# Kernel tuning notes

Measured on AMD Instinct MI355X. Metric: run time of the kernel, lower is better.

The kernel has to match this reference:

```python
import jax, jax.numpy as jnp
import numpy as np

N_PIECES = 20  # hard-coded in FSEncoderSized.__init__ (FSPool(..., 20))


def conv1x1(x, w, b):
    # x: (B, Cin, N), w: (Cout, Cin), b: (Cout,) -> (B, Cout, N)
    return jnp.einsum('bcn,dc->bdn', x, w) + b[None, :, None]


def fspool(x, weight):
    # x: (B, C, N); weight: (C, N_PIECES+1)
    # FSPool with n=None: sizes = arange(N)/(N-1) clamped to 1, mask all ones.
    B, C, N = x.shape
    ratio = jnp.clip(jnp.arange(N, dtype=jnp.float32) / max(N - 1, 1), 0.0, 1.0)
    pos = N_PIECES * ratio                      # (N,) in [0, N_PIECES]
    idx = jnp.floor(pos).astype(jnp.int32)
    frac = pos - idx
    left = weight[:, idx]                       # (C, N)
    right = weight[:, jnp.clip(idx + 1, 0, N_PIECES)]
    w = (1.0 - frac)[None, :] * left + frac[None, :] * right  # (C, N)
    xs = -jnp.sort(-x, axis=2)                  # descending sort along set dim
    return jnp.sum(xs * w[None], axis=2)        # (B, C)


def setup_inputs() -> dict:
    key = jax.random.key(0)
    ks = jax.random.split(key, 12)
    B, Cin, N = 1024, 5, 512
    dim, Cout = 256, 129
    C = Cout - 1  # 128
    x = jax.random.normal(ks[0], (B, Cin, N), dtype=jnp.float32)
    mask = (jax.random.uniform(ks[1], (B, N)) < 0.8).astype(jnp.float32)

    def kaiming(k, co, ci):
        return jax.random.normal(k, (co, ci), dtype=jnp.float32) * np.sqrt(2.0 / ci)

    w1 = kaiming(ks[2], dim, Cin); b1 = jnp.zeros((dim,), jnp.float32)
    w2 = kaiming(ks[3], dim, dim); b2 = jnp.zeros((dim,), jnp.float32)
    w3 = kaiming(ks[4], dim, dim); b3 = jnp.zeros((dim,), jnp.float32)
    w4 = kaiming(ks[5], C, dim);   b4 = jnp.zeros((C,), jnp.float32)
    pool_w = jax.random.normal(ks[6], (C, N_PIECES + 1), dtype=jnp.float32) * 0.1
    return {'x': x, 'mask': mask, 'w1': w1, 'b1': b1, 'w2': w2, 'b2': b2,
            'w3': w3, 'b3': b3, 'w4': w4, 'b4': b4, 'pool_w': pool_w}


def reference(x, mask, w1, b1, w2, b2, w3, b3, w4, b4, pool_w):
    m = mask[:, None, :]                         # (B, 1, N)
    h = jax.nn.relu(conv1x1(x, w1, b1))
    h = jax.nn.relu(conv1x1(h, w2, b2))
    h = jax.nn.relu(conv1x1(h, w3, b3))
    h = conv1x1(h, w4, b4)                       # (B, C, N)
    h = h / h.shape[2]                           # x / x.size(2)
    h = h * m
    pooled = fspool(h, pool_w)                   # (B, C)
    size_feat = jnp.mean(m, axis=2) * 4.0        # (B, 1)
    return jnp.concatenate([pooled, size_feat], axis=1)  # (B, C+1)
```

## Files before the change

### kernel.cpp

```cpp
#include <hip/hip_runtime.h>
#include <hip/hip_bf16.h>

typedef __bf16 bf16x8 __attribute__((ext_vector_type(8)));
typedef float f32x4 __attribute__((ext_vector_type(4)));
typedef unsigned short ushort_t;

#define NPOS 512
#define CIN  5
#define CO   128

static __device__ __forceinline__ unsigned short f2bf(float f){
  union { __hip_bfloat16 h; unsigned short u; } cv;
  cv.h = __float2bfloat16(f);
  return cv.u;
}

static __device__ __forceinline__ unsigned cvtpk_u32(float a, float b){
  union { __hip_bfloat162 h2; unsigned u; } cv;
  cv.h2 = __float22bfloat162_rn(make_float2(a, b));
  return cv.u;
}

static __device__ __forceinline__ unsigned pk_min_u16(unsigned a, unsigned b){
  unsigned d; asm("v_pk_min_u16 %0, %1, %2" : "=v"(d) : "v"(a), "v"(b)); return d;
}
static __device__ __forceinline__ unsigned pk_max_u16(unsigned a, unsigned b){
  unsigned d; asm("v_pk_max_u16 %0, %1, %2" : "=v"(d) : "v"(a), "v"(b)); return d;
}
static __device__ __forceinline__ unsigned pk_max_i16(unsigned a, unsigned b){
  unsigned d; asm("v_pk_max_i16 %0, %1, %2" : "=v"(d) : "v"(a), "v"(b)); return d;
}

template<int CTRL>
static __device__ __forceinline__ unsigned mov_dpp_u32(unsigned v){
  return (unsigned)__builtin_amdgcn_mov_dpp((int)v, CTRL, 0xf, 0xf, true);
}
template<int CTRL>
static __device__ __forceinline__ float fadd_dpp(float s){
  union {float f; int i;} u; u.f = s;
  union {int i; float f;} q; q.i = __builtin_amdgcn_mov_dpp(u.i, CTRL, 0xf, 0xf, true);
  return s + q.f;
}

__global__ void k_prep(const float* __restrict__ w1, const float* __restrict__ w2,
                       const float* __restrict__ w3, const float* __restrict__ w4,
                       const float* __restrict__ pw,
                       ushort_t* __restrict__ o, float* __restrict__ Wt){
  int i = blockIdx.x*256 + threadIdx.x;
  if (i < 65536)        o[i] = f2bf(w2[i]);
  else if (i < 131072)  o[i] = f2bf(w3[i-65536]);
  else if (i < 163840)  o[i] = f2bf(w4[i-131072]);
  else if (i < 172032){
    int j = i - 163840;
    int d = j >> 5, k = j & 31;
    o[i] = (k < CIN) ? f2bf(w1[d*CIN + k]) : (ushort_t)0;
  } else {
    int j = i - 172032;
    int c = j >> 9, ii = j & 511;
    int rk = 511 - ii;
    float pos = (float)rk * (20.0f/511.0f);
    int idx = (int)pos; if (idx > 20) idx = 20;
    float frac = pos - (float)idx;
    int i2 = (idx+1 > 20) ? 20 : idx+1;
    float wl = pw[c*21 + idx], wr = pw[c*21 + i2];
    Wt[c*512 + ii] = wl + frac*(wr - wl);
  }
}


template<int NSD, int KSTR>
static __device__ __forceinline__ void preload_w(bf16x8 (&wr)[3][4],
    const ushort_t* __restrict__ Wb, int slot, int ks, int wave, int lane){
  const int m = lane & 15, quad = lane >> 4;
  const int d0 = wave * (NSD*16);
  #pragma unroll
  for (int sd=0; sd<NSD; sd++)
    wr[slot][sd] = *(const bf16x8*)(Wb + (d0 + sd*16 + m)*KSTR + ks*32 + quad*8);
}

template<int NSD, int NKS>
static __device__ __forceinline__ void mfma_layer2(bf16x8 (&wr)[3][4],
    const ushort_t* __restrict__ Wb,
    const ushort_t* __restrict__ A0, const ushort_t* __restrict__ A1,
    const float* __restrict__ bias,
    f32x4 (&c0)[4][4], f32x4 (&c1)[4][4], int wave, int lane){
  const int m = lane & 15;
  #pragma unroll
  for (int sd=0;sd<NSD;sd++){
    float bv = bias[wave*(NSD*16) + sd*16 + m];
    f32x4 bvv = (f32x4){bv,bv,bv,bv};
    #pragma unroll
    for (int sn=0;sn<4;sn++){ c0[sn][sd] = bvv; c1[sn][sd] = bvv; }
  }
  #pragma unroll
  for (int ks=0; ks<NKS; ks++){
    if (ks+2 < NKS) preload_w<NSD,256>(wr, Wb, (ks+2)%3, ks+2, wave, lane);
    bf16x8 a0[4], a1[4];
    #pragma unroll
    for (int sn=0;sn<4;sn++){
      a0[sn] = *(const bf16x8*)(A0 + ((sn*512 + ks*64 + lane) << 3));
      a1[sn] = *(const bf16x8*)(A1 + ((sn*512 + ks*64 + lane) << 3));
    }
    #pragma unroll
    for (int sd=0;sd<NSD;sd++){
      #pragma unroll
      for (int sn=0;sn<4;sn++){
        c0[sn][sd] = __builtin_amdgcn_mfma_f32_16x16x32_bf16(a0[sn], wr[ks%3][sd], c0[sn][sd], 0,0,0);
        c1[sn][sd] = __builtin_amdgcn_mfma_f32_16x16x32_bf16(a1[sn], wr[ks%3][sd], c1[sn][sd], 0,0,0);
      }
    }
  }
}

static __device__ __forceinline__ void epilogue_relu(const f32x4 (&c)[4][4],
    ushort_t* __restrict__ dst, int wave, int lane){
  const int m = lane & 15, quad = lane >> 4;
  const int d0 = wave * 64;
  #pragma unroll
  for (int sd=0;sd<4;sd++){
    int d = d0 + sd*16 + m;
    int colbase = (d>>5)*64 + ((d>>3)&3)*16;
    int j = d & 7;
    #pragma unroll
    for (int sn=0;sn<4;sn++){
      unsigned u01 = pk_max_i16(cvtpk_u32(c[sn][sd][0], c[sn][sd][1]), 0u);
      unsigned u23 = pk_max_i16(cvtpk_u32(c[sn][sd][2], c[sn][sd][3]), 0u);
      int base = (sn*512 + colbase + quad*4) << 3;
      dst[base +  0 + j] = (ushort_t)u01;
      dst[base +  8 + j] = (ushort_t)(u01 >> 16);
      dst[base + 16 + j] = (ushort_t)u23;
      dst[base + 24 + j] = (ushort_t)(u23 >> 16);
    }
  }
}

__global__ __launch_bounds__(256,2) void k_fused(
  const float* __restrict__ x, const float* __restrict__ mask,
  const ushort_t* __restrict__ w1b, const float* __restrict__ b1,
  const ushort_t* __restrict__ w2b, const float* __restrict__ b2,
  const ushort_t* __restrict__ w3b, const float* __restrict__ b3,
  const ushort_t* __restrict__ w4b, const float* __restrict__ b4,
  ushort_t* __restrict__ h4)
{
  __shared__ __align__(16) ushort_t Act0[64*256];
  __shared__ __align__(16) ushort_t Act1[64*256];
  const int t    = threadIdx.x;
  const int bid  = blockIdx.x;
  const int b    = bid >> 2;
  const int n0   = (bid & 3) << 7;
  const int wave = t >> 6, lane = t & 63;

  bf16x8 wr[3][4];
  f32x4  c0[4][4], c1[4][4];

  {
    const int sn = t >> 6, col = (t >> 4) & 3, n16 = t & 15;
    uint4 u0 = make_uint4(0u,0u,0u,0u), u1 = u0;
    if (col == 0){
      const float* xp = x + (size_t)b*CIN*NPOS + n0 + sn*16 + n16;
      u0.x = cvtpk_u32(xp[0],      xp[NPOS]);
      u0.y = cvtpk_u32(xp[2*NPOS], xp[3*NPOS]);
      u0.z = cvtpk_u32(xp[4*NPOS], 0.f);
      const float* xq = xp + 64;
      u1.x = cvtpk_u32(xq[0],      xq[NPOS]);
      u1.y = cvtpk_u32(xq[2*NPOS], xq[3*NPOS]);
      u1.z = cvtpk_u32(xq[4*NPOS], 0.f);
    }
    *(uint4*)&Act0[(sn*512 + col*16 + n16) << 3] = u0;
    *(uint4*)&Act1[(sn*512 + col*16 + n16) << 3] = u1;
  }
  preload_w<4,32>(wr, w1b, 0, 0, wave, lane);
  __syncthreads();

  mfma_layer2<4,1>(wr, w1b, Act0, Act1, b1, c0, c1, wave, lane);
  preload_w<4,256>(wr, w2b, 0, 0, wave, lane);
  preload_w<4,256>(wr, w2b, 1, 1, wave, lane);
  __syncthreads();
  epilogue_relu(c0, Act0, wave, lane);
  epilogue_relu(c1, Act1, wave, lane);
  __syncthreads();

  mfma_layer2<4,8>(wr, w2b, Act0, Act1, b2, c0, c1, wave, lane);
  preload_w<4,256>(wr, w3b, 0, 0, wave, lane);
  preload_w<4,256>(wr, w3b, 1, 1, wave, lane);
  __syncthreads();
  epilogue_relu(c0, Act0, wave, lane);
  epilogue_relu(c1, Act1, wave, lane);
  __syncthreads();

  mfma_layer2<4,8>(wr, w3b, Act0, Act1, b3, c0, c1, wave, lane);
  preload_w<2,256>(wr, w4b, 0, 0, wave, lane);
  preload_w<2,256>(wr, w4b, 1, 1, wave, lane);
  __syncthreads();
  epilogue_relu(c0, Act0, wave, lane);
  epilogue_relu(c1, Act1, wave, lane);
  __syncthreads();

  mfma_layer2<2,8>(wr, w4b, Act0, Act1, b4, c0, c1, wave, lane);
  {
    const int m = lane & 15, quad = lane >> 4;
    const float* mk = mask + (size_t)b*NPOS + n0;
    #pragma unroll
    for (int sd=0;sd<2;sd++){
      const int d = wave*32 + sd*16 + m;
      ushort_t* rowp = h4 + ((size_t)b*CO + d)*NPOS + n0;
      #pragma unroll
      for (int sn=0;sn<4;sn++){
        float4 mr0 = *(const float4*)(mk + sn*16 + quad*4);
        float4 mr1 = *(const float4*)(mk + 64 + sn*16 + quad*4);
        unsigned q0 = cvtpk_u32(c0[sn][sd][0] * (1.0f/512.0f) * mr0.x,
                                c0[sn][sd][1] * (1.0f/512.0f) * mr0.y);
        unsigned q1 = cvtpk_u32(c0[sn][sd][2] * (1.0f/512.0f) * mr0.z,
                                c0[sn][sd][3] * (1.0f/512.0f) * mr0.w);
        *(uint2*)(rowp + sn*16 + quad*4) = make_uint2(q0, q1);
        unsigned p0 = cvtpk_u32(c1[sn][sd][0] * (1.0f/512.0f) * mr1.x,
                                c1[sn][sd][1] * (1.0f/512.0f) * mr1.y);
        unsigned p1 = cvtpk_u32(c1[sn][sd][2] * (1.0f/512.0f) * mr1.z,
                                c1[sn][sd][3] * (1.0f/512.0f) * mr1.w);
        *(uint2*)(rowp + 64 + sn*16 + quad*4) = make_uint2(p0, p1);
      }
    }
  }
}


static __device__ __forceinline__ void ce_up(unsigned &a, unsigned &b){
  unsigned mn = pk_min_u16(a,b), mx = pk_max_u16(a,b); a = mn; b = mx;
}
static __device__ __forceinline__ void ce_dn(unsigned &a, unsigned &b){
  unsigned mn = pk_min_u16(a,b), mx = pk_max_u16(a,b); a = mx; b = mn;
}
static __device__ __forceinline__ void clean8(unsigned (&v)[8]){
  ce_up(v[0],v[4]); ce_up(v[1],v[5]); ce_up(v[2],v[6]); ce_up(v[3],v[7]);
  ce_up(v[0],v[2]); ce_up(v[1],v[3]); ce_up(v[4],v[6]); ce_up(v[5],v[7]);
  ce_up(v[0],v[1]); ce_up(v[2],v[3]); ce_up(v[4],v[5]); ce_up(v[6],v[7]);
}
static __device__ __forceinline__ void flip8(unsigned (&v)[8], unsigned f){
  #pragma unroll
  for (int i=0;i<8;i++) v[i] ^= f;
}
template<int CTRL>
static __device__ __forceinline__ void xr_dpp(unsigned (&v)[8], bool low){
  #pragma unroll
  for (int i=0;i<8;i++){
    unsigned p = mov_dpp_u32<CTRL>(v[i]);
    unsigned mn = pk_min_u16(v[i], p), mx = pk_max_u16(v[i], p);
    v[i] = low ? mn : mx;
  }
}
static __device__ __forceinline__ void xr_shfl(unsigned (&v)[8], int lm, bool low){
  #pragma unroll
  for (int i=0;i<8;i++){
    unsigned p = (unsigned)__shfl_xor((int)v[i], lm);
    unsigned mn = pk_min_u16(v[i], p), mx = pk_max_u16(v[i], p);
    v[i] = low ? mn : mx;
  }
}

__global__ void k_pool(const ushort_t* __restrict__ h4, const float* __restrict__ Wt,
                       float* __restrict__ out)
{
  const int lane = threadIdx.x & 63;
  const int wave = threadIdx.x >> 6;
  const size_t r0 = (size_t)blockIdx.x*8 + wave*2;
  const int b0 = (int)(r0 >> 7), c0 = (int)(r0 & 127);
  const int b1_ = (int)((r0+1) >> 7), c1 = (int)((r0+1) & 127);

  uint4 ra = *(const uint4*)(h4 + r0*NPOS     + lane*8);
  uint4 rb = *(const uint4*)(h4 + (r0+1)*NPOS + lane*8);

  unsigned v[8];
  v[0] = (ra.x & 0xFFFFu) | (rb.x << 16);
  v[1] = (ra.x >> 16)     | (rb.x & 0xFFFF0000u);
  v[2] = (ra.y & 0xFFFFu) | (rb.y << 16);
  v[3] = (ra.y >> 16)     | (rb.y & 0xFFFF0000u);
  v[4] = (ra.z & 0xFFFFu) | (rb.z << 16);
  v[5] = (ra.z >> 16)     | (rb.z & 0xFFFF0000u);
  v[6] = (ra.w & 0xFFFFu) | (rb.w << 16);
  v[7] = (ra.w >> 16)     | (rb.w & 0xFFFF0000u);

  #pragma unroll
  for (int i=0;i<8;i++){
    unsigned sb = (v[i] >> 15) & 0x00010001u;
    v[i] = v[i] ^ 0x80008000u ^ (sb * 0x7FFFu);
  }

  const bool lo1  = (lane & 1)  == 0;
  const bool lo2  = (lane & 2)  == 0;
  const bool lo4  = (lane & 4)  == 0;
  const bool lo8  = (lane & 8)  == 0;
  const bool lo16 = (lane & 16) == 0;
  const bool lo32 = (lane & 32) == 0;

  const unsigned F8   = (lane & 1)  ? 0xFFFFFFFFu : 0u;
  const unsigned F16  = (lane & 2)  ? 0xFFFFFFFFu : 0u;
  const unsigned F32  = (lane & 4)  ? 0xFFFFFFFFu : 0u;
  const unsigned F64  = (lane & 8)  ? 0xFFFFFFFFu : 0u;
  const unsigned F128 = (lane & 16) ? 0xFFFFFFFFu : 0u;
  const unsigned F256 = (lane & 32) ? 0xFFFFFFFFu : 0u;

  ce_up(v[0],v[1]); ce_dn(v[2],v[3]); ce_up(v[4],v[5]); ce_dn(v[6],v[7]);
  ce_up(v[0],v[2]); ce_up(v[1],v[3]); ce_dn(v[4],v[6]); ce_dn(v[5],v[7]);
  ce_up(v[0],v[1]); ce_up(v[2],v[3]); ce_dn(v[4],v[5]); ce_dn(v[6],v[7]);

  flip8(v, F8);
  clean8(v);
  flip8(v, F8 ^ F16);
  xr_dpp<0xB1>(v, lo1);
  clean8(v);
  flip8(v, F16 ^ F32);
  xr_dpp<0x4E>(v, lo2); xr_dpp<0xB1>(v, lo1);
  clean8(v);
  flip8(v, F32 ^ F64);
  xr_shfl(v, 4, lo4); xr_dpp<0x4E>(v, lo2); xr_dpp<0xB1>(v, lo1);
  clean8(v);
  flip8(v, F64 ^ F128);
  xr_dpp<0x128>(v, lo8); xr_shfl(v, 4, lo4); xr_dpp<0x4E>(v, lo2); xr_dpp<0xB1>(v, lo1);
  clean8(v);
  flip8(v, F128 ^ F256);
  xr_shfl(v, 16, lo16); xr_dpp<0x128>(v, lo8); xr_shfl(v, 4, lo4);
  xr_dpp<0x4E>(v, lo2); xr_dpp<0xB1>(v, lo1);
  clean8(v);
  flip8(v, F256);
  xr_shfl(v, 32, lo32); xr_shfl(v, 16, lo16); xr_dpp<0x128>(v, lo8);
  xr_shfl(v, 4, lo4); xr_dpp<0x4E>(v, lo2); xr_dpp<0xB1>(v, lo1);
  clean8(v);

  #pragma unroll
  for (int i=0;i<8;i++){
    unsigned sb = ((~v[i]) >> 15) & 0x00010001u;
    v[i] = v[i] ^ 0x80008000u ^ (sb * 0x7FFFu);
  }

  float w0[8], w1a[8];
  *(float4*)&w0[0]  = *(const float4*)(Wt + c0*512 + lane*8);
  *(float4*)&w0[4]  = *(const float4*)(Wt + c0*512 + lane*8 + 4);
  *(float4*)&w1a[0] = *(const float4*)(Wt + c1*512 + lane*8);
  *(float4*)&w1a[4] = *(const float4*)(Wt + c1*512 + lane*8 + 4);

  float s0 = 0.f, s1 = 0.f;
  #pragma unroll
  for (int i=0;i<8;i++){
    union {unsigned u; float f;} lo, hi;
    lo.u = v[i] << 16;
    hi.u = v[i] & 0xFFFF0000u;
    s0 = fmaf(lo.f, w0[i],  s0);
    s1 = fmaf(hi.f, w1a[i], s1);
  }
  s0 = fadd_dpp<0xB1>(s0);  s1 = fadd_dpp<0xB1>(s1);
  s0 = fadd_dpp<0x4E>(s0);  s1 = fadd_dpp<0x4E>(s1);
  s0 = fadd_dpp<0x128>(s0); s1 = fadd_dpp<0x128>(s1);
  s0 += __shfl_xor(s0, 4);  s1 += __shfl_xor(s1, 4);
  s0 += __shfl_xor(s0, 16); s1 += __shfl_xor(s1, 16);
  s0 += __shfl_xor(s0, 32); s1 += __shfl_xor(s1, 32);

  if (lane == 0){
    out[b0*129 + c0]  = s0;
    out[b1_*129 + c1] = s1;
  }
}

__global__ void k_size(const float* __restrict__ mask, float* __restrict__ out){
  const int b = blockIdx.x, lane = threadIdx.x;
  float s = 0.f;
  #pragma unroll
  for (int i=0;i<8;i++) s += mask[(size_t)b*NPOS + i*64 + lane];
  #pragma unroll
  for (int off=32; off>=1; off>>=1) s += __shfl_xor(s, off);
  if (lane == 0) out[b*129 + 128] = s * (1.0f/128.0f);
}

extern "C" void kernel_launch(void* const* d_in, const int* in_sizes, int n_in,
                              void* d_out, int out_size, void* d_ws, size_t ws_size,
                              hipStream_t stream){
  const float* x    = (const float*)d_in[0];
  const float* mask = (const float*)d_in[1];
  const float* w1   = (const float*)d_in[2];
  const float* b1   = (const float*)d_in[3];
  const float* w2   = (const float*)d_in[4];
  const float* b2   = (const float*)d_in[5];
  const float* w3   = (const float*)d_in[6];
  const float* b3   = (const float*)d_in[7];
  const float* w4   = (const float*)d_in[8];
  const float* b4   = (const float*)d_in[9];
  const float* pw   = (const float*)d_in[10];
  float* out = (float*)d_out;

  ushort_t* h4  = (ushort_t*)d_ws;
  ushort_t* w2b = h4 + (size_t)1024*CO*NPOS;
  ushort_t* w3b = w2b + 65536;
  ushort_t* w4b = w3b + 65536;
  ushort_t* w1b = w4b + 32768;
  float*    Wt  = (float*)(w1b + 8192);

  k_prep <<<928,   256, 0, stream>>>(w1, w2, w3, w4, pw, w2b, Wt);
  k_fused<<<4096,  256, 0, stream>>>(x, mask, w1b, b1, w2b, b2, w3b, b3, w4b, b4, h4);
  k_pool <<<16384, 256, 0, stream>>>(h4, Wt, out);
  k_size <<<1024,  64,  0, stream>>>(mask, out);
}
```

Before: 393.9 us.

## Swap MFMA operand order for vectorized LDS epilogue and fold size into pool

Hidden layers now compute with weights as the A operand and activations as B, so each lane holds four consecutive output channels. The ReLU epilogue can then write 8-byte packed stores to LDS instead of four scalar 2-byte stores. The bias is loaded as a float4 per lane. Separately, the mask-size reduction is folded into the first 1024 blocks of k_pool, which removes one kernel launch at the cost of slightly more work in those blocks.

```diff
diff --git a/kernel.cpp b/kernel.cpp
--- a/kernel.cpp
+++ b/kernel.cpp
@@ -78,33 +78,66 @@
     wr[slot][sd] = *(const bf16x8*)(Wb + (d0 + sd*16 + m)*KSTR + ks*32 + quad*8);
 }
 
-template<int NSD, int NKS>
-static __device__ __forceinline__ void mfma_layer2(bf16x8 (&wr)[3][4],
+template<int NKS>
+static __device__ __forceinline__ void mfma_WA(bf16x8 (&wr)[3][4],
+    const ushort_t* __restrict__ Wb,
+    const ushort_t* __restrict__ A0, const ushort_t* __restrict__ A1,
+    const float* __restrict__ bias,
+    f32x4 (&c0)[4][4], f32x4 (&c1)[4][4], int wave, int lane){
+  const int quad = lane >> 4;
+  #pragma unroll
+  for (int db=0; db<4; db++){
+    float4 b4v = *(const float4*)(bias + wave*64 + db*16 + quad*4);
+    f32x4 bvv = (f32x4){b4v.x, b4v.y, b4v.z, b4v.w};
+    #pragma unroll
+    for (int nb=0; nb<4; nb++){ c0[nb][db] = bvv; c1[nb][db] = bvv; }
+  }
+  #pragma unroll
+  for (int ks=0; ks<NKS; ks++){
+    if (ks+2 < NKS) preload_w<4,256>(wr, Wb, (ks+2)%3, ks+2, wave, lane);
+    bf16x8 a0[4], a1[4];
+    #pragma unroll
+    for (int nb=0; nb<4; nb++){
+      a0[nb] = *(const bf16x8*)(A0 + ((nb*512 + ks*64 + lane) << 3));
+      a1[nb] = *(const bf16x8*)(A1 + ((nb*512 + ks*64 + lane) << 3));
+    }
+    #pragma unroll
+    for (int db=0; db<4; db++){
+      #pragma unroll
+      for (int nb=0; nb<4; nb++){
+        c0[nb][db] = __builtin_amdgcn_mfma_f32_16x16x32_bf16(wr[ks%3][db], a0[nb], c0[nb][db], 0,0,0);
+        c1[nb][db] = __builtin_amdgcn_mfma_f32_16x16x32_bf16(wr[ks%3][db], a1[nb], c1[nb][db], 0,0,0);
+      }
+    }
+  }
+}
+
+static __device__ __forceinline__ void mfma_L4(bf16x8 (&wr)[3][4],
     const ushort_t* __restrict__ Wb,
     const ushort_t* __restrict__ A0, const ushort_t* __restrict__ A1,
     const float* __restrict__ bias,
     f32x4 (&c0)[4][4], f32x4 (&c1)[4][4], int wave, int lane){
   const int m = lane & 15;
   #pragma unroll
-  for (int sd=0;sd<NSD;sd++){
-    float bv = bias[wave*(NSD*16) + sd*16 + m];
+  for (int sd=0; sd<2; sd++){
+    float bv = bias[wave*32 + sd*16 + m];
     f32x4 bvv = (f32x4){bv,bv,bv,bv};
     #pragma unroll
-    for (int sn=0;sn<4;sn++){ c0[sn][sd] = bvv; c1[sn][sd] = bvv; }
-  }
-  #pragma unroll
-  for (int ks=0; ks<NKS; ks++){
-    if (ks+2 < NKS) preload_w<NSD,256>(wr, Wb, (ks+2)%3, ks+2, wave, lane);
+    for (int sn=0; sn<4; sn++){ c0[sn][sd] = bvv; c1[sn][sd] = bvv; }
+  }
+  #pragma unroll
+  for (int ks=0; ks<8; ks++){
+    if (ks+2 < 8) preload_w<2,256>(wr, Wb, (ks+2)%3, ks+2, wave, lane);
     bf16x8 a0[4], a1[4];
     #pragma unroll
-    for (int sn=0;sn<4;sn++){
+    for (int sn=0; sn<4; sn++){
       a0[sn] = *(const bf16x8*)(A0 + ((sn*512 + ks*64 + lane) << 3));
       a1[sn] = *(const bf16x8*)(A1 + ((sn*512 + ks*64 + lane) << 3));
     }
     #pragma unroll
-    for (int sd=0;sd<NSD;sd++){
+    for (int sd=0; sd<2; sd++){
       #pragma unroll
-      for (int sn=0;sn<4;sn++){
+      for (int sn=0; sn<4; sn++){
         c0[sn][sd] = __builtin_amdgcn_mfma_f32_16x16x32_bf16(a0[sn], wr[ks%3][sd], c0[sn][sd], 0,0,0);
         c1[sn][sd] = __builtin_amdgcn_mfma_f32_16x16x32_bf16(a1[sn], wr[ks%3][sd], c1[sn][sd], 0,0,0);
       }
@@ -115,21 +148,17 @@
 static __device__ __forceinline__ void epilogue_relu(const f32x4 (&c)[4][4],
     ushort_t* __restrict__ dst, int wave, int lane){
   const int m = lane & 15, quad = lane >> 4;
-  const int d0 = wave * 64;
-  #pragma unroll
-  for (int sd=0;sd<4;sd++){
-    int d = d0 + sd*16 + m;
-    int colbase = (d>>5)*64 + ((d>>3)&3)*16;
-    int j = d & 7;
-    #pragma unroll
-    for (int sn=0;sn<4;sn++){
-      unsigned u01 = pk_max_i16(cvtpk_u32(c[sn][sd][0], c[sn][sd][1]), 0u);
-      unsigned u23 = pk_max_i16(cvtpk_u32(c[sn][sd][2], c[sn][sd][3]), 0u);
-      int base = (sn*512 + colbase + quad*4) << 3;
-      dst[base +  0 + j] = (ushort_t)u01;
-      dst[base +  8 + j] = (ushort_t)(u01 >> 16);
-      dst[base + 16 + j] = (ushort_t)u23;
-      dst[base + 24 + j] = (ushort_t)(u23 >> 16);
+  #pragma unroll
+  for (int db=0; db<4; db++){
+    int cb    = wave*64 + db*16 + quad*4;
+    int colpt = (cb>>5)*64 + ((cb>>3)&3)*16;
+    int half  = (quad & 1) ? 4 : 0;
+    #pragma unroll
+    for (int nb=0; nb<4; nb++){
+      unsigned u01 = pk_max_i16(cvtpk_u32(c[nb][db][0], c[nb][db][1]), 0u);
+      unsigned u23 = pk_max_i16(cvtpk_u32(c[nb][db][2], c[nb][db][3]), 0u);
+      int chunk = nb*512 + colpt + m;
+      *(uint2*)&dst[(chunk << 3) + half] = make_uint2(u01, u23);
     }
   }
 }
@@ -172,7 +201,7 @@
   preload_w<4,32>(wr, w1b, 0, 0, wave, lane);
   __syncthreads();
 
-  mfma_layer2<4,1>(wr, w1b, Act0, Act1, b1, c0, c1, wave, lane);
+  mfma_WA<1>(wr, w1b, Act0, Act1, b1, c0, c1, wave, lane);
   preload_w<4,256>(wr, w2b, 0, 0, wave, lane);
   preload_w<4,256>(wr, w2b, 1, 1, wave, lane);
   __syncthreads();
@@ -180,7 +209,7 @@
   epilogue_relu(c1, Act1, wave, lane);
   __syncthreads();
 
-  mfma_layer2<4,8>(wr, w2b, Act0, Act1, b2, c0, c1, wave, lane);
+  mfma_WA<8>(wr, w2b, Act0, Act1, b2, c0, c1, wave, lane);
   preload_w<4,256>(wr, w3b, 0, 0, wave, lane);
   preload_w<4,256>(wr, w3b, 1, 1, wave, lane);
   __syncthreads();
@@ -188,7 +217,7 @@
   epilogue_relu(c1, Act1, wave, lane);
   __syncthreads();
 
-  mfma_layer2<4,8>(wr, w3b, Act0, Act1, b3, c0, c1, wave, lane);
+  mfma_WA<8>(wr, w3b, Act0, Act1, b3, c0, c1, wave, lane);
   preload_w<2,256>(wr, w4b, 0, 0, wave, lane);
   preload_w<2,256>(wr, w4b, 1, 1, wave, lane);
   __syncthreads();
@@ -196,7 +225,7 @@
   epilogue_relu(c1, Act1, wave, lane);
   __syncthreads();
 
-  mfma_layer2<2,8>(wr, w4b, Act0, Act1, b4, c0, c1, wave, lane);
+  mfma_L4(wr, w4b, Act0, Act1, b4, c0, c1, wave, lane);
   {
     const int m = lane & 15, quad = lane >> 4;
     const float* mk = mask + (size_t)b*NPOS + n0;
@@ -258,7 +287,7 @@
 }
 
 __global__ void k_pool(const ushort_t* __restrict__ h4, const float* __restrict__ Wt,
-                       float* __restrict__ out)
+                       const float* __restrict__ mask, float* __restrict__ out)
 {
   const int lane = threadIdx.x & 63;
   const int wave = threadIdx.x >> 6;
@@ -358,16 +387,19 @@
     out[b0*129 + c0]  = s0;
     out[b1_*129 + c1] = s1;
   }
-}
-
-__global__ void k_size(const float* __restrict__ mask, float* __restrict__ out){
-  const int b = blockIdx.x, lane = threadIdx.x;
-  float s = 0.f;
-  #pragma unroll
-  for (int i=0;i<8;i++) s += mask[(size_t)b*NPOS + i*64 + lane];
-  #pragma unroll
-  for (int off=32; off>=1; off>>=1) s += __shfl_xor(s, off);
-  if (lane == 0) out[b*129 + 128] = s * (1.0f/128.0f);
+
+  if (blockIdx.x < 1024 && wave == 0){
+    const int b = blockIdx.x;
+    float s = 0.f;
+    #pragma unroll
+    for (int i=0;i<2;i++){
+      float4 mv = *(const float4*)(mask + (size_t)b*NPOS + lane*8 + i*4);
+      s += mv.x + mv.y + mv.z + mv.w;
+    }
+    s = fadd_dpp<0xB1>(s); s = fadd_dpp<0x4E>(s); s = fadd_dpp<0x128>(s);
+    s += __shfl_xor(s, 4); s += __shfl_xor(s, 16); s += __shfl_xor(s, 32);
+    if (lane == 0) out[b*129 + 128] = s * (1.0f/128.0f);
+  }
 }
 
 extern "C" void kernel_launch(void* const* d_in, const int* in_sizes, int n_in,
@@ -395,6 +427,5 @@
 
   k_prep <<<928,   256, 0, stream>>>(w1, w2, w3, w4, pw, w2b, Wt);
   k_fused<<<4096,  256, 0, stream>>>(x, mask, w1b, b1, w2b, b2, w3b, b3, w4b, b4, h4);
-  k_pool <<<16384, 256, 0, stream>>>(h4, Wt, out);
-  k_size <<<1024,  64,  0, stream>>>(mask, out);
-}
+  k_pool <<<16384, 256, 0, stream>>>(h4, Wt, mask, out);
+}
```

Measured after the change: 374.6 us. 1.05x faster.
